# Optimization experiments

Hardware: AMD Instinct MI355X
Metric: run time of the kernel (lower is better)

Reference implementation:

```python
import jax, jax.numpy as jnp
import numpy as np

B, S, D = 16, 2048, 1024
E2 = 2 * 2048  # embed_dim * 2 FFN hidden
EPS = 1e-5


def layernorm(x, g, b):
    mu = jnp.mean(x, axis=-1, keepdims=True)
    var = jnp.mean(jnp.square(x - mu), axis=-1, keepdims=True)
    return (x - mu) * jax.lax.rsqrt(var + EPS) * g + b


def setup_inputs() -> dict:
    key = jax.random.key(0)
    ks = jax.random.split(key, 4)
    lags = jax.random.normal(ks[0], (B, S, D), dtype=jnp.float32)
    W1 = jax.random.normal(ks[1], (D, E2), dtype=jnp.float32) * (1.0 / np.sqrt(D))
    b1 = jnp.zeros((E2,), dtype=jnp.float32)
    W2 = jax.random.normal(ks[2], (E2, D), dtype=jnp.float32) * (1.0 / np.sqrt(E2))
    b2 = jnp.zeros((D,), dtype=jnp.float32)
    g1 = jnp.ones((D,), dtype=jnp.float32)
    be1 = jnp.zeros((D,), dtype=jnp.float32)
    g3 = jnp.ones((D,), dtype=jnp.float32)
    be3 = jnp.zeros((D,), dtype=jnp.float32)
    return {"lags": lags, "W1": W1, "b1": b1, "W2": W2, "b2": b2,
            "g1": g1, "be1": be1, "g3": g3, "be3": be3}


def reference(lags, W1, b1, W2, b2, g1, be1, g3, be3):
    # manual self-attention: scores = lags @ lags^T / sqrt(D)  -> [B,S,S]
    scale = 1.0 / jnp.sqrt(jnp.asarray(D, dtype=lags.dtype))
    scores = jnp.einsum('bsd,btd->bst', lags, lags) * scale
    attn = jax.nn.softmax(scores, axis=-1)
    attn_out = jnp.einsum('bst,btd->bsd', attn, lags)  # [B,S,D]
    x = layernorm(lags + attn_out, g1, be1)
    # FFN: Linear -> exact GELU -> Linear (dropout=0)
    h = jax.nn.gelu(jnp.einsum('bsd,de->bse', x, W1) + b1, approximate=False)
    ff = jnp.einsum('bse,ed->bsd', h, W2) + b2
    return layernorm(x + ff, g3, be3)
```

## Files before the change

### kernel.cpp

```cpp
#include <hip/hip_runtime.h>
#include <hip/hip_bf16.h>
#include <cmath>


typedef __bf16 bf16;
typedef __attribute__((ext_vector_type(8))) __bf16 bf16x8;
typedef __attribute__((ext_vector_type(4))) __bf16 bf16x4;
typedef __attribute__((ext_vector_type(4))) float f32x4;

static constexpr int kB  = 16;
static constexpr int kS  = 2048;
static constexpr int kD  = 1024;
static constexpr int kE2 = 4096;
static constexpr int kCB = 8;
static constexpr int kFR = 16384;

__device__ __forceinline__ void gload_lds16(const bf16* g, bf16* l) {
    __builtin_amdgcn_global_load_lds(
        (const __attribute__((address_space(1))) void*)g,
        (__attribute__((address_space(3))) void*)l,
        16, 0, 0);
}

__global__ __launch_bounds__(256) void cvt_bf16_kernel(const float* __restrict__ in,
                                                       bf16* __restrict__ out) {
    size_t i = ((size_t)blockIdx.x * 256 + threadIdx.x) * 4;
    float4 v = *(const float4*)(in + i);
    bf16x4 o;
    o.x = (bf16)v.x; o.y = (bf16)v.y; o.z = (bf16)v.z; o.w = (bf16)v.w;
    *(bf16x4*)(out + i) = o;
}

__global__ void transpose_cvt_kernel(const float* __restrict__ in, bf16* __restrict__ out,
                                     int R, int C, long long sIn, long long sOut) {
    __shared__ float tile[32][33];
    in  += (size_t)blockIdx.z * sIn;
    out += (size_t)blockIdx.z * sOut;
    const int c0 = blockIdx.x * 32, r0 = blockIdx.y * 32;
    const int tx = threadIdx.x, ty = threadIdx.y;
#pragma unroll
    for (int k = 0; k < 32; k += 8)
        tile[ty + k][tx] = in[(size_t)(r0 + ty + k) * C + (c0 + tx)];
    __syncthreads();
#pragma unroll
    for (int k = 0; k < 32; k += 8)
        out[(size_t)(c0 + ty + k) * R + (r0 + tx)] = (bf16)tile[tx][ty + k];
}

template <int MODE>
__global__ __launch_bounds__(512, 2)
void gemm_bt_kernel(const bf16* __restrict__ A, const bf16* __restrict__ Bm,
                    float* __restrict__ C, bf16* __restrict__ Cb,
                    const float* __restrict__ bias,
                    const float* __restrict__ resF, const bf16* __restrict__ resB,
                    int N, int K,
                    long long sA, long long sB, long long sC, long long sRes,
                    float scale) {
    __shared__ __align__(16) bf16 lds[2][2][2][256 * 32];
    bf16* Lb = &lds[0][0][0][0];
    const int tid  = threadIdx.x;
    const int lane = tid & 63;
    const int wv   = tid >> 6;
    const int wm   = wv >> 2;
    const int wn   = wv & 3;
    const int quad = lane >> 4, l15 = lane & 15;
    const int quadS = quad ^ ((l15 >> 1) & 3);

    const unsigned gx = gridDim.x, gy = gridDim.y;
    unsigned lin = blockIdx.x + gx * (blockIdx.y + gy * blockIdx.z);
    const unsigned nper = (gx * gy * gridDim.z) >> 3;
    lin = (lin & 7) * nper + (lin >> 3);
    const unsigned bx = lin % gx;
    const unsigned tq = lin / gx;
    const unsigned by = tq % gy;
    const long long z = tq / gy;

    const bf16* Ab = A  + z * sA + (size_t)by * 256 * K;
    const bf16* Bb = Bm + z * sB + (size_t)bx * 256 * K;

    const int srow = wv * 32 + (lane >> 2);
    const int scol = ((lane & 3) ^ ((lane >> 3) & 3)) * 8;
    const bf16* gA = Ab + (size_t)srow * K + scol;
    const bf16* gB = Bb + (size_t)srow * K + scol;
    const size_t kk16 = (size_t)16 * K;
    const int NTH = K >> 7;

    const bf16* aP = Lb + ((wm * 128 + l15) * 32 + quadS * 8);
    const bf16* bP = Lb + 16384 + ((wn * 64 + l15) * 32 + quadS * 8);
    bf16* ldsW = Lb + wv * 1024;

    f32x4 acc[8][4];
#pragma unroll
    for (int i = 0; i < 8; i++)
#pragma unroll
        for (int j = 0; j < 4; j++) {
            f32x4 zv = {0.0f, 0.0f, 0.0f, 0.0f};
            acc[i][j] = zv;
        }

#define STG(GT, SEL, BUF)                                                     \
    do {                                                                      \
        const bf16* g_ = (((SEL) & 1) ? (GT##B) : (GT##A)) + ((SEL) >> 1) * 32; \
        bf16* l_ = ldsW + (BUF) * 32768 + ((SEL) & 1) * 16384 + ((SEL) >> 1) * 8192; \
        gload_lds16(g_, l_);                                                  \
        gload_lds16(g_ + kk16, l_ + 512);                                     \
    } while (0)

#define VMC4 asm volatile("s_waitcnt vmcnt(4)" ::: "memory")
#define VMC0 asm volatile("s_waitcnt vmcnt(0)" ::: "memory")

#define GPHASE(BUF, KS, QM, READB, STG_STMT, WAIT_STMT)                       \
    do {                                                                      \
        if (READB) {                                                          \
            _Pragma("unroll")                                                 \
            for (int nf = 0; nf < 4; nf++)                                    \
                bfr[nf] = *(const bf16x8*)(bP + (BUF) * 32768 + (KS) * 8192 + nf * 512); \
        }                                                                     \
        _Pragma("unroll")                                                     \
        for (int mf = 0; mf < 4; mf++)                                        \
            afr[mf] = *(const bf16x8*)(aP + (BUF) * 32768 + (KS) * 8192 + ((QM) * 4 + mf) * 512); \
        STG_STMT;                                                             \
        asm volatile("" ::: "memory");                                        \
        __builtin_amdgcn_s_barrier();                                         \
        asm volatile("s_waitcnt lgkmcnt(0)" ::: "memory");                    \
        __builtin_amdgcn_sched_barrier(0);                                    \
        __builtin_amdgcn_s_setprio(1);                                        \
        _Pragma("unroll")                                                     \
        for (int mf = 0; mf < 4; mf++)                                        \
            _Pragma("unroll")                                                 \
            for (int nf = 0; nf < 4; nf++)                                    \
                acc[(QM) * 4 + mf][nf] = __builtin_amdgcn_mfma_f32_16x16x32_bf16( \
                    afr[mf], bfr[nf], acc[(QM) * 4 + mf][nf], 0, 0, 0);       \
        __builtin_amdgcn_s_setprio(0);                                        \
        WAIT_STMT;                                                            \
        __builtin_amdgcn_s_barrier();                                        \
        asm volatile("" ::: "memory");                                        \
    } while (0)

    bf16x8 afr[4], bfr[4];
    {
        const bf16* t0A = gA;      const bf16* t0B = gB;
        const bf16* t1A = gA + 64; const bf16* t1B = gB + 64;
        STG(t0, 0, 0); STG(t0, 1, 0); STG(t0, 2, 0); STG(t0, 3, 0);
        STG(t1, 0, 1); STG(t1, 1, 1);
        VMC4;
        __builtin_amdgcn_s_barrier();
        asm volatile("" ::: "memory");
    }

    for (int i = 0; i < NTH - 1; i++) {
        const bf16* t1A = gA + (size_t)(2 * i + 1) * 64;
        const bf16* t1B = gB + (size_t)(2 * i + 1) * 64;
        const bf16* t2A = t1A + 64;  const bf16* t2B = t1B + 64;
        const bf16* t3A = t1A + 128; const bf16* t3B = t1B + 128;
        GPHASE(0, 0, 0, true,  STG(t1, 2, 1), (void)0);
        GPHASE(0, 0, 1, false, STG(t1, 3, 1), (void)0);
        GPHASE(0, 1, 0, true,  STG(t2, 0, 0), (void)0);
        GPHASE(0, 1, 1, false, STG(t2, 1, 0), VMC4);
        GPHASE(1, 0, 0, true,  STG(t2, 2, 0), (void)0);
        GPHASE(1, 0, 1, false, STG(t2, 3, 0), (void)0);
        GPHASE(1, 1, 0, true,  STG(t3, 0, 1), (void)0);
        GPHASE(1, 1, 1, false, STG(t3, 1, 1), VMC4);
    }
    {
        const int i = NTH - 1;
        const bf16* t1A = gA + (size_t)(2 * i + 1) * 64;
        const bf16* t1B = gB + (size_t)(2 * i + 1) * 64;
        GPHASE(0, 0, 0, true,  STG(t1, 2, 1), (void)0);
        GPHASE(0, 0, 1, false, STG(t1, 3, 1), (void)0);
        GPHASE(0, 1, 0, true,  (void)0, (void)0);
        GPHASE(0, 1, 1, false, (void)0, VMC0);
        GPHASE(1, 0, 0, true,  (void)0, (void)0);
        GPHASE(1, 0, 1, false, (void)0, (void)0);
        GPHASE(1, 1, 0, true,  (void)0, (void)0);
        GPHASE(1, 1, 1, false, (void)0, (void)0);
    }
#undef GPHASE
#undef STG
#undef VMC4
#undef VMC0

    const size_t m0 = (size_t)by * 256 + wm * 128;
    const size_t n0 = (size_t)bx * 256 + wn * 64;
#pragma unroll
    for (int nf = 0; nf < 4; nf++) {
        const size_t col = n0 + nf * 16 + l15;
        const float bcol = (MODE == 2 || MODE == 3) ? bias[col] : 0.0f;
#pragma unroll
        for (int mf = 0; mf < 8; mf++) {
#pragma unroll
            for (int rr = 0; rr < 4; rr++) {
                const size_t row = m0 + mf * 16 + quad * 4 + rr;
                const float v = acc[mf][nf][rr];
                if (MODE == 0) {
                    Cb[z * sC + row * N + col] = (bf16)(v * scale);
                } else if (MODE == 1) {
                    C[z * sC + row * N + col] = v + resF[z * sRes + row * N + col];
                } else if (MODE == 2) {
                    const float t = v + bcol;
                    const float gl = 0.5f * t * (1.0f + erff(t * 0.70710678118654752f));
                    Cb[row * N + col] = (bf16)gl;
                } else {
                    C[row * N + col] = v + bcol + (float)resB[row * N + col];
                }
            }
        }
    }
}

__global__ __launch_bounds__(256)
void softmax_bf16_kernel(bf16* __restrict__ SP) {
    __shared__ float red[8];
    const size_t row = blockIdx.x;
    bf16* p = SP + row * kS;
    const int tid = threadIdx.x;
    bf16x8 v = *(const bf16x8*)(p + tid * 8);
    float f[8];
#pragma unroll
    for (int i = 0; i < 8; i++) f[i] = (float)v[i];
    float m = f[0];
#pragma unroll
    for (int i = 1; i < 8; i++) m = fmaxf(m, f[i]);
#pragma unroll
    for (int o = 32; o > 0; o >>= 1) m = fmaxf(m, __shfl_down(m, o, 64));
    if ((tid & 63) == 0) red[tid >> 6] = m;
    __syncthreads();
    m = fmaxf(fmaxf(red[0], red[1]), fmaxf(red[2], red[3]));
    float e[8], s = 0.0f;
#pragma unroll
    for (int i = 0; i < 8; i++) { e[i] = __expf(f[i] - m); s += e[i]; }
#pragma unroll
    for (int o = 32; o > 0; o >>= 1) s += __shfl_down(s, o, 64);
    __syncthreads();
    if ((tid & 63) == 0) red[4 + (tid >> 6)] = s;
    __syncthreads();
    s = red[4] + red[5] + red[6] + red[7];
    const float inv = 1.0f / s;
    bf16x8 o;
#pragma unroll
    for (int i = 0; i < 8; i++) o[i] = (bf16)(e[i] * inv);
    *(bf16x8*)(p + tid * 8) = o;
}

__global__ __launch_bounds__(256)
void layernorm_kernel(const float* __restrict__ in, const float* __restrict__ g,
                      const float* __restrict__ be, float* __restrict__ outF,
                      bf16* __restrict__ outB) {
    __shared__ float red[8];
    const size_t row = blockIdx.x;
    const float* src = in + row * kD;
    const int tid = threadIdx.x;
    float4 v = *(const float4*)(src + tid * 4);
    float s = v.x + v.y + v.z + v.w;
#pragma unroll
    for (int o = 32; o > 0; o >>= 1) s += __shfl_down(s, o, 64);
    if ((tid & 63) == 0) red[tid >> 6] = s;
    __syncthreads();
    const float mu = (red[0] + red[1] + red[2] + red[3]) * (1.0f / kD);
    const float d0 = v.x - mu, d1 = v.y - mu, d2 = v.z - mu, d3 = v.w - mu;
    float ss = d0 * d0 + d1 * d1 + d2 * d2 + d3 * d3;
#pragma unroll
    for (int o = 32; o > 0; o >>= 1) ss += __shfl_down(ss, o, 64);
    __syncthreads();
    if ((tid & 63) == 0) red[4 + (tid >> 6)] = ss;
    __syncthreads();
    const float var = (red[4] + red[5] + red[6] + red[7]) * (1.0f / kD);
    const float rstd = rsqrtf(var + 1e-5f);
    float4 gg = *(const float4*)(g + tid * 4);
    float4 bb = *(const float4*)(be + tid * 4);
    float4 o;
    o.x = d0 * rstd * gg.x + bb.x;
    o.y = d1 * rstd * gg.y + bb.y;
    o.z = d2 * rstd * gg.z + bb.z;
    o.w = d3 * rstd * gg.w + bb.w;
    if (outF) *(float4*)(outF + row * kD + tid * 4) = o;
    if (outB) {
        bf16x4 ob;
        ob.x = (bf16)o.x; ob.y = (bf16)o.y; ob.z = (bf16)o.z; ob.w = (bf16)o.w;
        *(bf16x4*)(outB + row * kD + tid * 4) = ob;
    }
}

extern "C" void kernel_launch(void* const* d_in, const int* in_sizes, int n_in,
                              void* d_out, int out_size, void* d_ws, size_t ws_size,
                              hipStream_t stream) {
    const float* lags = (const float*)d_in[0];
    const float* W1   = (const float*)d_in[1];
    const float* b1   = (const float*)d_in[2];
    const float* W2   = (const float*)d_in[3];
    const float* b2   = (const float*)d_in[4];
    const float* g1   = (const float*)d_in[5];
    const float* be1  = (const float*)d_in[6];
    const float* g3   = (const float*)d_in[7];
    const float* be3  = (const float*)d_in[8];
    float* out = (float*)d_out;

    const size_t REQUIRED = (size_t)(64 + 8 + 8 + 64 + 64) * 1024 * 1024;
    if (ws_size < REQUIRED) return;

    char* w = (char*)d_ws;
    bf16* lagsb = (bf16*)w; w += (size_t)kB * kS * kD * 2;
    bf16* W1T   = (bf16*)w; w += (size_t)kD * kE2 * 2;
    bf16* W2T   = (bf16*)w; w += (size_t)kE2 * kD * 2;
    bf16* lagsT = (bf16*)w; w += (size_t)kB * kD * kS * 2;
    bf16* SP    = (bf16*)w;
    bf16* xb    = lagsb;
    bf16* h     = lagsT;

    const int n = kB * kS * kD;

    cvt_bf16_kernel<<<n / 1024, 256, 0, stream>>>(lags, lagsb);
    transpose_cvt_kernel<<<dim3(kD / 32, kS / 32, kB), dim3(32, 8), 0, stream>>>(
        lags, lagsT, kS, kD, (long long)kS * kD, (long long)kD * kS);
    transpose_cvt_kernel<<<dim3(kE2 / 32, kD / 32, 1), dim3(32, 8), 0, stream>>>(
        W1, W1T, kD, kE2, 0, 0);
    transpose_cvt_kernel<<<dim3(kD / 32, kE2 / 32, 1), dim3(32, 8), 0, stream>>>(
        W2, W2T, kE2, kD, 0, 0);

    for (int c = 0; c < kB / kCB; c++) {
        const size_t off = (size_t)c * kCB * kS * kD;
        gemm_bt_kernel<0><<<dim3(kS / 256, kS / 256, kCB), 512, 0, stream>>>(
            lagsb + off, lagsb + off, nullptr, SP, nullptr, nullptr, nullptr,
            kS, kD, (long long)kS * kD, (long long)kS * kD, (long long)kS * kS, 0, 0.03125f);
        softmax_bf16_kernel<<<kCB * kS, 256, 0, stream>>>(SP);
        gemm_bt_kernel<1><<<dim3(kD / 256, kS / 256, kCB), 512, 0, stream>>>(
            SP, lagsT + off, out + off, nullptr, nullptr, lags + off, nullptr,
            kD, kS, (long long)kS * kS, (long long)kD * kS,
            (long long)kS * kD, (long long)kS * kD, 1.0f);
        layernorm_kernel<<<kCB * kS, 256, 0, stream>>>(out + off, g1, be1, nullptr, xb + off);
    }

    for (int c = 0; c < (kB * kS) / kFR; c++) {
        const size_t roff = (size_t)c * kFR * kD;
        gemm_bt_kernel<2><<<dim3(kE2 / 256, kFR / 256, 1), 512, 0, stream>>>(
            xb + roff, W1T, nullptr, h, b1, nullptr, nullptr,
            kE2, kD, 0, 0, 0, 0, 1.0f);
        gemm_bt_kernel<3><<<dim3(kD / 256, kFR / 256, 1), 512, 0, stream>>>(
            h, W2T, out + roff, nullptr, b2, nullptr, xb + roff,
            kD, kE2, 0, 0, 0, 0, 1.0f);
    }

    layernorm_kernel<<<kB * kS, 256, 0, stream>>>(out, g3, be3, out, nullptr);
}
```

Before: 1.417 ms.

## Prefetch next-phase LDS fragments into double-buffered registers in GEMM main loop

Restructures the GEMM phase pipeline so each phase issues the LDS reads for the next phase's A/B fragments before computing the current MFMAs, using double-buffered register fragments. The waits on lgkmcnt and vmcnt are relaxed to partial counts so LDS reads and global-to-LDS loads overlap with MFMA work instead of draining before each phase. This raises register pressure and depends on exact wait-count accounting across barriers, which risks hazards.

```diff
diff --git a/kernel.cpp b/kernel.cpp
--- a/kernel.cpp
+++ b/kernel.cpp
@@ -106,23 +106,32 @@
         gload_lds16(g_ + kk16, l_ + 512);                                     \
     } while (0)
 
-#define VMC4 asm volatile("s_waitcnt vmcnt(4)" ::: "memory")
+#define VMC6 asm volatile("s_waitcnt vmcnt(6)" ::: "memory")
 #define VMC0 asm volatile("s_waitcnt vmcnt(0)" ::: "memory")
 
-#define GPHASE(BUF, KS, QM, READB, STG_STMT, WAIT_STMT)                       \
+#define RDE(BUF, KS)                                                          \
     do {                                                                      \
-        if (READB) {                                                          \
-            _Pragma("unroll")                                                 \
-            for (int nf = 0; nf < 4; nf++)                                    \
-                bfr[nf] = *(const bf16x8*)(bP + (BUF) * 32768 + (KS) * 8192 + nf * 512); \
-        }                                                                     \
+        _Pragma("unroll")                                                     \
+        for (int nf = 0; nf < 4; nf++)                                        \
+            bfr[KS][nf] = *(const bf16x8*)(bP + (BUF) * 32768 + (KS) * 8192 + nf * 512); \
         _Pragma("unroll")                                                     \
         for (int mf = 0; mf < 4; mf++)                                        \
-            afr[mf] = *(const bf16x8*)(aP + (BUF) * 32768 + (KS) * 8192 + ((QM) * 4 + mf) * 512); \
+            afr[0][mf] = *(const bf16x8*)(aP + (BUF) * 32768 + (KS) * 8192 + mf * 512); \
+    } while (0)
+#define RDO(BUF, KS)                                                          \
+    do {                                                                      \
+        _Pragma("unroll")                                                     \
+        for (int mf = 0; mf < 4; mf++)                                        \
+            afr[1][mf] = *(const bf16x8*)(aP + (BUF) * 32768 + (KS) * 8192 + (4 + mf) * 512); \
+    } while (0)
+
+#define GPHASE(KS, QM, NEXTRD, STG_STMT, VM_STMT, LGN)                        \
+    do {                                                                      \
+        NEXTRD;                                                               \
         STG_STMT;                                                             \
         asm volatile("" ::: "memory");                                        \
         __builtin_amdgcn_s_barrier();                                         \
-        asm volatile("s_waitcnt lgkmcnt(0)" ::: "memory");                    \
+        asm volatile("s_waitcnt lgkmcnt(" #LGN ")" ::: "memory");             \
         __builtin_amdgcn_sched_barrier(0);                                    \
         __builtin_amdgcn_s_setprio(1);                                        \
         _Pragma("unroll")                                                     \
@@ -130,22 +139,23 @@
             _Pragma("unroll")                                                 \
             for (int nf = 0; nf < 4; nf++)                                    \
                 acc[(QM) * 4 + mf][nf] = __builtin_amdgcn_mfma_f32_16x16x32_bf16( \
-                    afr[mf], bfr[nf], acc[(QM) * 4 + mf][nf], 0, 0, 0);       \
+                    afr[QM][mf], bfr[KS][nf], acc[(QM) * 4 + mf][nf], 0, 0, 0); \
         __builtin_amdgcn_s_setprio(0);                                        \
-        WAIT_STMT;                                                            \
-        __builtin_amdgcn_s_barrier();                                        \
+        VM_STMT;                                                              \
+        __builtin_amdgcn_s_barrier();                                         \
         asm volatile("" ::: "memory");                                        \
     } while (0)
 
-    bf16x8 afr[4], bfr[4];
+    bf16x8 afr[2][4], bfr[2][4];
     {
         const bf16* t0A = gA;      const bf16* t0B = gB;
         const bf16* t1A = gA + 64; const bf16* t1B = gB + 64;
         STG(t0, 0, 0); STG(t0, 1, 0); STG(t0, 2, 0); STG(t0, 3, 0);
         STG(t1, 0, 1); STG(t1, 1, 1);
-        VMC4;
+        asm volatile("s_waitcnt vmcnt(8)" ::: "memory");
         __builtin_amdgcn_s_barrier();
         asm volatile("" ::: "memory");
+        RDE(0, 0);
     }
 
     for (int i = 0; i < NTH - 1; i++) {
@@ -153,31 +163,33 @@
         const bf16* t1B = gB + (size_t)(2 * i + 1) * 64;
         const bf16* t2A = t1A + 64;  const bf16* t2B = t1B + 64;
         const bf16* t3A = t1A + 128; const bf16* t3B = t1B + 128;
-        GPHASE(0, 0, 0, true,  STG(t1, 2, 1), (void)0);
-        GPHASE(0, 0, 1, false, STG(t1, 3, 1), (void)0);
-        GPHASE(0, 1, 0, true,  STG(t2, 0, 0), (void)0);
-        GPHASE(0, 1, 1, false, STG(t2, 1, 0), VMC4);
-        GPHASE(1, 0, 0, true,  STG(t2, 2, 0), (void)0);
-        GPHASE(1, 0, 1, false, STG(t2, 3, 0), (void)0);
-        GPHASE(1, 1, 0, true,  STG(t3, 0, 1), (void)0);
-        GPHASE(1, 1, 1, false, STG(t3, 1, 1), VMC4);
+        GPHASE(0, 0, RDO(0, 0), STG(t1, 2, 1), VMC6,    4);
+        GPHASE(0, 1, RDE(0, 1), STG(t1, 3, 1), (void)0, 8);
+        GPHASE(1, 0, RDO(0, 1), STG(t2, 0, 0), VMC6,    4);
+        GPHASE(1, 1, RDE(1, 0), STG(t2, 1, 0), (void)0, 8);
+        GPHASE(0, 0, RDO(1, 0), STG(t2, 2, 0), VMC6,    4);
+        GPHASE(0, 1, RDE(1, 1), STG(t2, 3, 0), (void)0, 8);
+        GPHASE(1, 0, RDO(1, 1), STG(t3, 0, 1), VMC6,    4);
+        GPHASE(1, 1, RDE(0, 0), STG(t3, 1, 1), (void)0, 8);
     }
     {
         const int i = NTH - 1;
         const bf16* t1A = gA + (size_t)(2 * i + 1) * 64;
         const bf16* t1B = gB + (size_t)(2 * i + 1) * 64;
-        GPHASE(0, 0, 0, true,  STG(t1, 2, 1), (void)0);
-        GPHASE(0, 0, 1, false, STG(t1, 3, 1), (void)0);
-        GPHASE(0, 1, 0, true,  (void)0, (void)0);
-        GPHASE(0, 1, 1, false, (void)0, VMC0);
-        GPHASE(1, 0, 0, true,  (void)0, (void)0);
-        GPHASE(1, 0, 1, false, (void)0, (void)0);
-        GPHASE(1, 1, 0, true,  (void)0, (void)0);
-        GPHASE(1, 1, 1, false, (void)0, (void)0);
+        GPHASE(0, 0, RDO(0, 0), STG(t1, 2, 1), VMC6,    4);
+        GPHASE(0, 1, RDE(0, 1), STG(t1, 3, 1), (void)0, 8);
+        GPHASE(1, 0, RDO(0, 1), (void)0,       VMC0,    4);
+        GPHASE(1, 1, RDE(1, 0), (void)0,       (void)0, 8);
+        GPHASE(0, 0, RDO(1, 0), (void)0,       (void)0, 4);
+        GPHASE(0, 1, RDE(1, 1), (void)0,       (void)0, 8);
+        GPHASE(1, 0, RDO(1, 1), (void)0,       (void)0, 4);
+        GPHASE(1, 1, (void)0,   (void)0,       (void)0, 0);
     }
 #undef GPHASE
+#undef RDE
+#undef RDO
 #undef STG
-#undef VMC4
+#undef VMC6
 #undef VMC0
 
     const size_t m0 = (size_t)by * 256 + wm * 128;
```

After: 1.461 ms. 1.03x slower.
